# Performance work log

Hardware: AMD Instinct MI355X
Metric: run time of the kernel (lower is better)

## Reference

```python
import jax, jax.numpy as jnp
import jax.scipy as jsp
import numpy as np

H, W, C = 2048, 2048, 3
SCALE, TRANSLATE, ROTATE, SHEAR = 1.15, 0.15, np.pi / 12, 0.0


def _rotation_matrix(r):
    rx, ry = jnp.cos(r), jnp.sin(r)
    return jnp.array([[rx, ry, 0.0], [-ry, rx, 0.0], [0.0, 0.0, 1.0]])


def _scale_matrix(s):
    return jnp.array([[s, 0.0, 0.0], [0.0, s, 0.0], [0.0, 0.0, 1.0]])


def _shear_matrix(r):
    sh = jnp.tan(r)
    return jnp.array([[1.0, sh, 0.0], [0.0, 1.0, 0.0], [0.0, 0.0, 1.0]])


def _translation_matrix(tx, ty):
    return jnp.array([[1.0, 0.0, tx], [0.0, 1.0, ty], [0.0, 0.0, 1.0]])


def setup_inputs() -> dict:
    key = jax.random.key(0)
    k_img, k1, k2, k3, k4, k5 = jax.random.split(key, 6)
    image = jax.random.normal(k_img, (H, W, C), dtype=jnp.float32)
    # Random affine params exactly as RandomAffine.__call__ samples them.
    scale = jax.random.uniform(k1, minval=1.0, maxval=SCALE)
    tx = jax.random.uniform(k2, minval=-TRANSLATE, maxval=TRANSLATE) * W
    ty = jax.random.uniform(k3, minval=-TRANSLATE, maxval=TRANSLATE) * H
    rotation = jax.random.uniform(k4, minval=-1.0, maxval=1.0) * ROTATE
    shear = jax.random.uniform(k5, minval=-1.0, maxval=1.0) * SHEAR
    matrix = (_rotation_matrix(rotation) @ _scale_matrix(scale)
              @ _shear_matrix(shear) @ _translation_matrix(tx, ty))
    return {"image": image, "matrix": matrix.astype(jnp.float32)}


def _apply_affine(image, matrix):
    h, w, c = image.shape
    dtype = image.dtype
    y = jnp.linspace(-h / 2, h / 2, num=h)
    x = jnp.linspace(-w / 2, w / 2, num=w)
    v = jnp.ones(1)
    ch = jnp.arange(3)
    # (h, w, 1, 3, 4) grid of homogeneous coords [y, x, 1, channel]
    coords = jnp.stack(jnp.meshgrid(y, x, v, ch, indexing='ij'), axis=-1).astype(dtype)
    transform = jnp.eye(4, dtype=dtype).at[:-1, :-1].set(matrix.astype(dtype))
    coords = coords @ transform + jnp.array([h / 2, w / 2, 0.0, 0.0], dtype=dtype)
    # drop the homogeneous slot (index -2), keep (y, x, channel)
    coords = jnp.concatenate([coords[..., :2], coords[..., 3:]], axis=-1)
    # 'h w v c yxc -> yxc (h w v c)'
    coords = coords.reshape(-1, 3).T  # (3, h*w*3)
    out = jsp.ndimage.map_coordinates(
        image, [coords[0], coords[1], coords[2]], order=1, mode='reflect')
    return out.reshape(h, w, c)


def reference(image, matrix):
    return _apply_affine(image, matrix)
```

## Files before the change

### kernel.cpp

```cpp
#include <hip/hip_runtime.h>


#define IMG_H 2048
#define IMG_W 2048
#define TH    16
#define TW    32
#define NT    8
#define BBH   32
#define NV4C  37
#define STR   (NV4C * 4)
#define BUFN  (BBH * STR)

__device__ __forceinline__ int reflect2048(int i) {
    int p = i & 4095;
    return (p < 2048) ? p : (4095 - p);
}

__device__ __forceinline__ void gl2lds16(const float* g, float* l) {
    __builtin_amdgcn_global_load_lds(
        (const __attribute__((address_space(1))) void*)g,
        (__attribute__((address_space(3))) void*)l,
        16, 0, 0);
}

__global__ __launch_bounds__(256) void affine_dbuf16_kernel(
    const float* __restrict__ img, const float* __restrict__ Mp,
    float* __restrict__ out)
{
    __shared__ float lds[2][BUFN];

    const int tid = threadIdx.x;
    const int grp = blockIdx.x & 7;
    const int tby = blockIdx.x >> 3;
    const int i0 = tby * TH;
    const int j0base = grp * (TW * NT);

    const float step = 2048.0f / 2047.0f;
    const float m00 = Mp[0], m01 = Mp[1];
    const float m10 = Mp[3], m11 = Mp[4];
    const float b0 = Mp[6] + 1024.0f, b1 = Mp[7] + 1024.0f;

    const float yv0 = fmaf((float)i0,          step, -1024.0f);
    const float yv1 = fmaf((float)(i0 + TH-1), step, -1024.0f);

    auto bbox = [&](int j0, int& y0, int& x0, int& nrows, int& nv4, bool& fast) {
        const float xva = fmaf((float)j0,        step, -1024.0f);
        const float xvb = fmaf((float)(j0+TW-1), step, -1024.0f);
        const float rya = yv0*m00 + xva*m10 + b0, ryb = yv0*m00 + xvb*m10 + b0;
        const float ryc = yv1*m00 + xva*m10 + b0, ryd = yv1*m00 + xvb*m10 + b0;
        const float rxa = yv0*m01 + xva*m11 + b1, rxb = yv0*m01 + xvb*m11 + b1;
        const float rxc = yv1*m01 + xva*m11 + b1, rxd = yv1*m01 + xvb*m11 + b1;
        const float miny = fminf(fminf(rya,ryb), fminf(ryc,ryd));
        const float maxy = fmaxf(fmaxf(rya,ryb), fmaxf(ryc,ryd));
        const float minx = fminf(fminf(rxa,rxb), fminf(rxc,rxd));
        const float maxx = fmaxf(fmaxf(rxa,rxb), fmaxf(rxc,rxd));
        y0 = (int)floorf(miny) - 1;
        nrows = (int)floorf(maxy) + 3 - y0;
        if (nrows > BBH) nrows = BBH;
        x0 = ((int)floorf(minx) - 1) & ~3;
        const int xw = (int)floorf(maxx) + 3 - x0;
        nv4 = (xw * 3 + 3) >> 2;
        if (nv4 > NV4C) nv4 = NV4C;
        fast = (x0 >= 0) && (x0*3 + nv4*4 <= IMG_W*3);
    };

    auto dmafill = [&](float* buf, int y0, int x0, int nrows, int nv4) {
        const int wid = tid >> 6, lane = tid & 63;
        if (lane < nv4) {
            for (int r = wid; r < nrows; r += 4) {
                const int gy = reflect2048(y0 + r);
                gl2lds16(img + gy*(IMG_W*3) + x0*3 + lane*4, &buf[r*STR]);
            }
        }
    };
    auto slowfill = [&](float* buf, int y0, int x0, int nrows) {
        for (int e = tid; e < nrows*48; e += 256) {
            const int r  = e / 48;
            const int xx = e - r*48;
            const int gy = reflect2048(y0 + r);
            const int gx = reflect2048(x0 + xx);
            const float* s = img + (gy*IMG_W + gx)*3;
            float* d = &buf[r*STR + xx*3];
            d[0] = s[0]; d[1] = s[1]; d[2] = s[2];
        }
    };

    auto compute = [&](const float* buf, int j0, int y0, int x0) {
        #pragma unroll
        for (int pass = 0; pass < 2; ++pass) {
            const int row = pass*8 + (tid >> 5);
            const int col = tid & 31;
            const int i = i0 + row, j = j0 + col;
            const float yv = fmaf((float)i, step, -1024.0f);
            const float xv = fmaf((float)j, step, -1024.0f);
            const float ry = yv*m00 + xv*m10 + b0;
            const float rx = yv*m01 + xv*m11 + b1;
            const float fy = floorf(ry), fx = floorf(rx);
            const float wy1 = ry - fy, wx1 = rx - fx;
            const float wy0 = 1.0f - wy1, wx0 = 1.0f - wx1;
            const int iy = (int)fy - y0;
            const int ix = (int)fx - x0;
            const float* p0 = &buf[iy*STR + ix*3];
            const float* p1 = p0 + STR;
            const float w00 = wy0*wx0, w01 = wy0*wx1;
            const float w10 = wy1*wx0, w11 = wy1*wx1;
            float* ob = out + (i*IMG_W + j)*3;
            ob[0] = w00*p0[0] + w01*p0[3] + w10*p1[0] + w11*p1[3];
            ob[1] = w00*p0[1] + w01*p0[4] + w10*p1[1] + w11*p1[4];
            ob[2] = w00*p0[2] + w01*p0[5] + w10*p1[2] + w11*p1[5];
        }
    };

    int y0c, x0c, nrc, nvc; bool fc;
    bbox(j0base, y0c, x0c, nrc, nvc, fc);
    if (fc) dmafill(lds[0], y0c, x0c, nrc, nvc);
    else    slowfill(lds[0], y0c, x0c, nrc);
    __syncthreads();

    int cur = 0;
    for (int t = 0; t < NT; ++t) {
        const int j0 = j0base + t*TW;
        int y0n, x0n, nrn, nvn; bool fn = false;
        if (t+1 < NT) {
            bbox(j0 + TW, y0n, x0n, nrn, nvn, fn);
            if (fn) dmafill(lds[cur^1], y0n, x0n, nrn, nvn);
            else    slowfill(lds[cur^1], y0n, x0n, nrn);
        }
        compute(lds[cur], j0, y0c, x0c);
        __syncthreads();
        y0c = y0n; x0c = x0n; cur ^= 1;
    }
}

extern "C" void kernel_launch(void* const* d_in, const int* in_sizes, int n_in,
                              void* d_out, int out_size, void* d_ws, size_t ws_size,
                              hipStream_t stream) {
    const float* img = (const float*)d_in[0];
    const float* M   = (const float*)d_in[1];
    float* out = (float*)d_out;

    dim3 grid((IMG_H / TH) * (IMG_W / (TW * NT))), block(256);
    hipLaunchKernelGGL(affine_dbuf16_kernel, grid, block, 0, stream, img, M, out);
}
```

Before: 113.7 us.

## Replace double-buffered tile loop with one tile per block for occupancy

Drops the per-block loop over eight horizontal tiles with double-buffered LDS prefetch. Each block now processes a single 16x32 output tile with a single LDS buffer, and the grid is eight times larger. The goal is to halve LDS per block and raise occupancy, relying on many resident blocks rather than explicit intra-block prefetch to hide latency. The cost is that fill and compute no longer overlap within a block, and there are more block launches and bounding-box setups.

```diff
diff --git a/kernel.cpp b/kernel.cpp
--- a/kernel.cpp
+++ b/kernel.cpp
@@ -5,7 +5,6 @@
 #define IMG_W 2048
 #define TH    16
 #define TW    32
-#define NT    8
 #define BBH   32
 #define NV4C  37
 #define STR   (NV4C * 4)
@@ -23,17 +22,16 @@
         16, 0, 0);
 }
 
-__global__ __launch_bounds__(256) void affine_dbuf16_kernel(
+__global__ __launch_bounds__(256) void affine_occ_kernel(
     const float* __restrict__ img, const float* __restrict__ Mp,
     float* __restrict__ out)
 {
-    __shared__ float lds[2][BUFN];
+    __shared__ float lds[BUFN];
 
     const int tid = threadIdx.x;
-    const int grp = blockIdx.x & 7;
-    const int tby = blockIdx.x >> 3;
-    const int i0 = tby * TH;
-    const int j0base = grp * (TW * NT);
+    const int tbx = blockIdx.x & 63;
+    const int tby = blockIdx.x >> 6;
+    const int i0 = tby * TH, j0 = tbx * TW;
 
     const float step = 2048.0f / 2047.0f;
     const float m00 = Mp[0], m01 = Mp[1];
@@ -42,93 +40,70 @@
 
     const float yv0 = fmaf((float)i0,          step, -1024.0f);
     const float yv1 = fmaf((float)(i0 + TH-1), step, -1024.0f);
+    const float xva = fmaf((float)j0,          step, -1024.0f);
+    const float xvb = fmaf((float)(j0 + TW-1), step, -1024.0f);
 
-    auto bbox = [&](int j0, int& y0, int& x0, int& nrows, int& nv4, bool& fast) {
-        const float xva = fmaf((float)j0,        step, -1024.0f);
-        const float xvb = fmaf((float)(j0+TW-1), step, -1024.0f);
-        const float rya = yv0*m00 + xva*m10 + b0, ryb = yv0*m00 + xvb*m10 + b0;
-        const float ryc = yv1*m00 + xva*m10 + b0, ryd = yv1*m00 + xvb*m10 + b0;
-        const float rxa = yv0*m01 + xva*m11 + b1, rxb = yv0*m01 + xvb*m11 + b1;
-        const float rxc = yv1*m01 + xva*m11 + b1, rxd = yv1*m01 + xvb*m11 + b1;
-        const float miny = fminf(fminf(rya,ryb), fminf(ryc,ryd));
-        const float maxy = fmaxf(fmaxf(rya,ryb), fmaxf(ryc,ryd));
-        const float minx = fminf(fminf(rxa,rxb), fminf(rxc,rxd));
-        const float maxx = fmaxf(fmaxf(rxa,rxb), fmaxf(rxc,rxd));
-        y0 = (int)floorf(miny) - 1;
-        nrows = (int)floorf(maxy) + 3 - y0;
-        if (nrows > BBH) nrows = BBH;
-        x0 = ((int)floorf(minx) - 1) & ~3;
-        const int xw = (int)floorf(maxx) + 3 - x0;
-        nv4 = (xw * 3 + 3) >> 2;
-        if (nv4 > NV4C) nv4 = NV4C;
-        fast = (x0 >= 0) && (x0*3 + nv4*4 <= IMG_W*3);
-    };
+    const float rya = yv0*m00 + xva*m10 + b0, ryb = yv0*m00 + xvb*m10 + b0;
+    const float ryc = yv1*m00 + xva*m10 + b0, ryd = yv1*m00 + xvb*m10 + b0;
+    const float rxa = yv0*m01 + xva*m11 + b1, rxb = yv0*m01 + xvb*m11 + b1;
+    const float rxc = yv1*m01 + xva*m11 + b1, rxd = yv1*m01 + xvb*m11 + b1;
 
-    auto dmafill = [&](float* buf, int y0, int x0, int nrows, int nv4) {
+    const float miny = fminf(fminf(rya,ryb), fminf(ryc,ryd));
+    const float maxy = fmaxf(fmaxf(rya,ryb), fmaxf(ryc,ryd));
+    const float minx = fminf(fminf(rxa,rxb), fminf(rxc,rxd));
+    const float maxx = fmaxf(fmaxf(rxa,rxb), fmaxf(rxc,rxd));
+
+    const int y0 = (int)floorf(miny) - 1;
+    int nrows = (int)floorf(maxy) + 3 - y0;
+    if (nrows > BBH) nrows = BBH;
+    const int x0 = ((int)floorf(minx) - 1) & ~3;
+    const int xw = (int)floorf(maxx) + 3 - x0;
+    int nv4 = (xw * 3 + 3) >> 2;
+    if (nv4 > NV4C) nv4 = NV4C;
+
+    if (x0 >= 0 && x0*3 + nv4*4 <= IMG_W*3) {
         const int wid = tid >> 6, lane = tid & 63;
         if (lane < nv4) {
             for (int r = wid; r < nrows; r += 4) {
                 const int gy = reflect2048(y0 + r);
-                gl2lds16(img + gy*(IMG_W*3) + x0*3 + lane*4, &buf[r*STR]);
+                gl2lds16(img + gy*(IMG_W*3) + x0*3 + lane*4, &lds[r*STR]);
             }
         }
-    };
-    auto slowfill = [&](float* buf, int y0, int x0, int nrows) {
+    } else {
         for (int e = tid; e < nrows*48; e += 256) {
             const int r  = e / 48;
             const int xx = e - r*48;
             const int gy = reflect2048(y0 + r);
             const int gx = reflect2048(x0 + xx);
             const float* s = img + (gy*IMG_W + gx)*3;
-            float* d = &buf[r*STR + xx*3];
+            float* d = &lds[r*STR + xx*3];
             d[0] = s[0]; d[1] = s[1]; d[2] = s[2];
         }
-    };
-
-    auto compute = [&](const float* buf, int j0, int y0, int x0) {
-        #pragma unroll
-        for (int pass = 0; pass < 2; ++pass) {
-            const int row = pass*8 + (tid >> 5);
-            const int col = tid & 31;
-            const int i = i0 + row, j = j0 + col;
-            const float yv = fmaf((float)i, step, -1024.0f);
-            const float xv = fmaf((float)j, step, -1024.0f);
-            const float ry = yv*m00 + xv*m10 + b0;
-            const float rx = yv*m01 + xv*m11 + b1;
-            const float fy = floorf(ry), fx = floorf(rx);
-            const float wy1 = ry - fy, wx1 = rx - fx;
-            const float wy0 = 1.0f - wy1, wx0 = 1.0f - wx1;
-            const int iy = (int)fy - y0;
-            const int ix = (int)fx - x0;
-            const float* p0 = &buf[iy*STR + ix*3];
-            const float* p1 = p0 + STR;
-            const float w00 = wy0*wx0, w01 = wy0*wx1;
-            const float w10 = wy1*wx0, w11 = wy1*wx1;
-            float* ob = out + (i*IMG_W + j)*3;
-            ob[0] = w00*p0[0] + w01*p0[3] + w10*p1[0] + w11*p1[3];
-            ob[1] = w00*p0[1] + w01*p0[4] + w10*p1[1] + w11*p1[4];
-            ob[2] = w00*p0[2] + w01*p0[5] + w10*p1[2] + w11*p1[5];
-        }
-    };
-
-    int y0c, x0c, nrc, nvc; bool fc;
-    bbox(j0base, y0c, x0c, nrc, nvc, fc);
-    if (fc) dmafill(lds[0], y0c, x0c, nrc, nvc);
-    else    slowfill(lds[0], y0c, x0c, nrc);
+    }
     __syncthreads();
 
-    int cur = 0;
-    for (int t = 0; t < NT; ++t) {
-        const int j0 = j0base + t*TW;
-        int y0n, x0n, nrn, nvn; bool fn = false;
-        if (t+1 < NT) {
-            bbox(j0 + TW, y0n, x0n, nrn, nvn, fn);
-            if (fn) dmafill(lds[cur^1], y0n, x0n, nrn, nvn);
-            else    slowfill(lds[cur^1], y0n, x0n, nrn);
-        }
-        compute(lds[cur], j0, y0c, x0c);
-        __syncthreads();
-        y0c = y0n; x0c = x0n; cur ^= 1;
+    #pragma unroll
+    for (int pass = 0; pass < 2; ++pass) {
+        const int row = pass*8 + (tid >> 5);
+        const int col = tid & 31;
+        const int i = i0 + row, j = j0 + col;
+        const float yv = fmaf((float)i, step, -1024.0f);
+        const float xv = fmaf((float)j, step, -1024.0f);
+        const float ry = yv*m00 + xv*m10 + b0;
+        const float rx = yv*m01 + xv*m11 + b1;
+        const float fy = floorf(ry), fx = floorf(rx);
+        const float wy1 = ry - fy, wx1 = rx - fx;
+        const float wy0 = 1.0f - wy1, wx0 = 1.0f - wx1;
+        const int iy = (int)fy - y0;
+        const int ix = (int)fx - x0;
+        const float* p0 = &lds[iy*STR + ix*3];
+        const float* p1 = p0 + STR;
+        const float w00 = wy0*wx0, w01 = wy0*wx1;
+        const float w10 = wy1*wx0, w11 = wy1*wx1;
+        float* ob = out + (i*IMG_W + j)*3;
+        ob[0] = w00*p0[0] + w01*p0[3] + w10*p1[0] + w11*p1[3];
+        ob[1] = w00*p0[1] + w01*p0[4] + w10*p1[1] + w11*p1[4];
+        ob[2] = w00*p0[2] + w01*p0[5] + w10*p1[2] + w11*p1[5];
     }
 }
 
@@ -139,6 +114,6 @@
     const float* M   = (const float*)d_in[1];
     float* out = (float*)d_out;
 
-    dim3 grid((IMG_H / TH) * (IMG_W / (TW * NT))), block(256);
-    hipLaunchKernelGGL(affine_dbuf16_kernel, grid, block, 0, stream, img, M, out);
+    dim3 grid((IMG_H / TH) * (IMG_W / TW)), block(256);
+    hipLaunchKernelGGL(affine_occ_kernel, grid, block, 0, stream, img, M, out);
 }
```

New measurement: 103.8 us. -8.7%, faster.
